# Optimization experiments

Measured on AMD Instinct MI355X. Metric: run time of the kernel, lower is better.

Reference implementation:

```python
import jax, jax.numpy as jnp
import numpy as np

N_NODES = 100000
N_EDGES = 1600000
IN_CH = 128
HEADS = 4
OUT_CH = 32
NEG_SLOPE = 0.2
DIV_WEIGHT = 0.1
EPS_SOFTMAX = 1e-16  # PyG softmax eps
EPS_COS = 1e-8       # F.cosine_similarity eps


def setup_inputs() -> dict:
    key = jax.random.key(0)
    k1, k2, k3, k4, k5 = jax.random.split(key, 5)
    x = jax.random.normal(k1, (N_NODES, IN_CH), dtype=jnp.float32)
    # edge_index with guaranteed no self loops (remove_self_loops becomes a no-op)
    row = jax.random.randint(k2, (N_EDGES,), 0, N_NODES, dtype=jnp.int32)
    off = jax.random.randint(k3, (N_EDGES,), 1, N_NODES, dtype=jnp.int32)
    col = (row + off) % N_NODES
    edge_index = jnp.stack([row, col], axis=0)
    # params (xavier-ish scale)
    W = jax.random.normal(k4, (HEADS * OUT_CH, IN_CH), dtype=jnp.float32) * np.sqrt(2.0 / (IN_CH + HEADS * OUT_CH))
    att = jax.random.normal(k5, (1, HEADS, 2 * OUT_CH), dtype=jnp.float32) * np.sqrt(2.0 / (1 + 2 * OUT_CH))
    bias = jnp.zeros((HEADS * OUT_CH,), dtype=jnp.float32)
    return {"x": x, "edge_index": edge_index, "W": W, "att": att, "bias": bias}


def reference(x, edge_index, W, att, bias):
    N = x.shape[0]
    H = att.shape[1]
    C = att.shape[2] // 2
    idx_dtype = edge_index.dtype
    # add self loops (input has none, so remove_self_loops is a no-op)
    loops = jnp.arange(N, dtype=idx_dtype)
    row = jnp.concatenate([edge_index[0], loops])  # destination
    col = jnp.concatenate([edge_index[1], loops])  # source
    # linear projection -> [N, H, C]
    h = (x @ W.T).reshape(N, H, C)
    # attention logits: (cat(x_i, x_j) * att).sum(-1) == s_i[row] + s_j[col]
    s_i = jnp.einsum('nhc,hc->nh', h, att[0, :, :C])  # [N, H]
    s_j = jnp.einsum('nhc,hc->nh', h, att[0, :, C:])  # [N, H]
    e = s_i[row] + s_j[col]                            # [E, H]
    e = jnp.where(e >= 0, e, NEG_SLOPE * e)            # leaky_relu
    # segment softmax over destination node (row)
    e_max = jax.ops.segment_max(e, row, num_segments=N)
    e_max = jnp.where(jnp.isfinite(e_max), e_max, 0.0)
    e_exp = jnp.exp(e - e_max[row])
    denom = jax.ops.segment_sum(e_exp, row, num_segments=N)
    alpha = e_exp / (denom[row] + EPS_SOFTMAX)         # [E, H]
    # attention diversity loss: mean pairwise cosine sim (zero diagonal)
    gram = alpha.T @ alpha                             # [H, H]
    norms = jnp.sqrt(jnp.diag(gram))
    corr = gram / jnp.maximum(norms[:, None] * norms[None, :], EPS_COS)
    corr = corr * (1.0 - jnp.eye(H, dtype=corr.dtype))
    diversity_loss = jnp.mean(corr) * DIV_WEIGHT
    # weighted message + scatter-add aggregation (dropout p=0 -> identity)
    msg = h[col] * alpha[:, :, None]                   # [E, H, C]
    out = jax.ops.segment_sum(msg, row, num_segments=N)
    out = out.reshape(N, H * C) + bias                 # concat=True
    return out, diversity_loss
```

## Files before the change

kernel.cpp:

```cpp
#include <hip/hip_runtime.h>
#include <math.h>

#define HC     128
#define SLOT   64
#define AGG_BLOCKS 2048
#define NPART  8
#define CHUNKS 256

typedef unsigned int uint32;
typedef short bf16x8 __attribute__((ext_vector_type(8)));
typedef float f32x4 __attribute__((ext_vector_type(4)));

__device__ inline unsigned short f2bf(float f){
  uint32 u = __float_as_uint(f);
  u = (u + 0x7fffu + ((u >> 16) & 1u)) >> 16;
  return (unsigned short)u;
}
__device__ inline uint32 pack_bf2(float a, float b){
  return (uint32)f2bf(a) | ((uint32)f2bf(b) << 16);
}
__device__ inline void lds_fence(){
  asm volatile("s_waitcnt lgkmcnt(0)" ::: "memory");
  __builtin_amdgcn_sched_barrier(0);
}


__global__ __launch_bounds__(256) void k_fill(const int* __restrict__ row, const int* __restrict__ col,
                                              int* cnt, int* bucket, int E, int N){
  int k = blockIdx.x & (NPART-1);
  int c = blockIdx.x >> 3;
  int per  = (E + CHUNKS - 1) / CHUNKS;
  int base = c * per;
  int end  = base + per; if (end > E) end = E;
  int rng  = (N + NPART - 1) / NPART;
  int lo = k * rng, hi = lo + rng;
  for (int i = base + threadIdx.x; i < end; i += 256){
    int d = row[i];
    if (d >= lo && d < hi){
      int pos = atomicAdd(&cnt[d], 1);
      if (pos < SLOT-1) bucket[(size_t)d*SLOT + pos] = col[i];
    }
  }
}


__global__ __launch_bounds__(256) void k_gemm(const float* __restrict__ x, const float* __restrict__ W,
                                              const float* __restrict__ att,
                                              uint32* __restrict__ h_pair,
                                              float* __restrict__ s_i, float* __restrict__ s_j, int N){
  __shared__ __align__(16) unsigned short Blds[128*128];
  int t = threadIdx.x;
  int w = t >> 6, l = t & 63;
  int o = l & 15, lg = l >> 4;
  int n0 = blockIdx.x * 64;

  #pragma unroll
  for (int i = 0; i < 8; ++i){
    int id = t + i*256;
    int r  = id >> 4, ck = id & 15;
    int sw = ck ^ (r & 7);
    float4 b0 = *(const float4*)&W[(size_t)r*128 + ck*8];
    float4 b1 = *(const float4*)&W[(size_t)r*128 + ck*8 + 4];
    bf16x8 pb;
    pb[0]=(short)f2bf(b0.x); pb[1]=(short)f2bf(b0.y); pb[2]=(short)f2bf(b0.z); pb[3]=(short)f2bf(b0.w);
    pb[4]=(short)f2bf(b1.x); pb[5]=(short)f2bf(b1.y); pb[6]=(short)f2bf(b1.z); pb[7]=(short)f2bf(b1.w);
    *(bf16x8*)&Blds[r*128 + sw*8] = pb;
  }

  int arow = n0 + w*16 + o;
  bool rok = (arow < N);
  const float* xr = x + (size_t)arow*128;
  bf16x8 afr[4];
  #pragma unroll
  for (int ks = 0; ks < 4; ++ks){
    float4 a0 = make_float4(0.f,0.f,0.f,0.f), a1 = a0;
    if (rok){
      a0 = *(const float4*)&xr[ks*32 + lg*8];
      a1 = *(const float4*)&xr[ks*32 + lg*8 + 4];
    }
    bf16x8 pa;
    pa[0]=(short)f2bf(a0.x); pa[1]=(short)f2bf(a0.y); pa[2]=(short)f2bf(a0.z); pa[3]=(short)f2bf(a0.w);
    pa[4]=(short)f2bf(a1.x); pa[5]=(short)f2bf(a1.y); pa[6]=(short)f2bf(a1.z); pa[7]=(short)f2bf(a1.w);
    afr[ks] = pa;
  }
  __syncthreads();

  f32x4 acc[8];
  #pragma unroll
  for (int cf = 0; cf < 8; ++cf) acc[cf] = (f32x4){0.f,0.f,0.f,0.f};

  #pragma unroll
  for (int ks = 0; ks < 4; ++ks){
    int ckk = ks*4 + lg;
    #pragma unroll
    for (int cf = 0; cf < 8; ++cf){
      int rb = cf*16 + o;
      bf16x8 bfr = *(const bf16x8*)&Blds[rb*128 + (ckk ^ (rb & 7))*8];
      acc[cf] = __builtin_amdgcn_mfma_f32_16x16x32_bf16(afr[ks], bfr, acc[cf], 0, 0, 0);
    }
  }

  float ai0[4], ai1[4], aj0[4], aj1[4];
  #pragma unroll
  for (int hd = 0; hd < 4; ++hd){
    ai0[hd] = att[hd*64 + o];
    ai1[hd] = att[hd*64 + 16 + o];
    aj0[hd] = att[hd*64 + 32 + o];
    aj1[hd] = att[hd*64 + 48 + o];
  }

  #pragma unroll
  for (int q = 0; q < 4; ++q){
    int node = n0 + w*16 + lg*4 + q;
    float v[8];
    #pragma unroll
    for (int cf = 0; cf < 8; ++cf) v[cf] = acc[cf][q];
    float pi[4], pj[4];
    #pragma unroll
    for (int hd = 0; hd < 4; ++hd){
      pi[hd] = v[2*hd]*ai0[hd] + v[2*hd+1]*ai1[hd];
      pj[hd] = v[2*hd]*aj0[hd] + v[2*hd+1]*aj1[hd];
    }
    #pragma unroll
    for (int sh = 1; sh < 16; sh <<= 1){
      #pragma unroll
      for (int hd = 0; hd < 4; ++hd){
        pi[hd] += __shfl_xor(pi[hd], sh);
        pj[hd] += __shfl_xor(pj[hd], sh);
      }
    }
    if (node < N){
      #pragma unroll
      for (int hd = 0; hd < 4; ++hd)
        h_pair[(size_t)node*64 + hd*16 + o] = pack_bf2(v[2*hd], v[2*hd+1]);
      if (o == 0){
        *(float4*)&s_i[(size_t)node*4] = make_float4(pi[0], pi[1], pi[2], pi[3]);
        *(float4*)&s_j[(size_t)node*4] = make_float4(pj[0], pj[1], pj[2], pj[3]);
      }
    }
  }
}


__global__ __launch_bounds__(256) void k_agg(const uint32* __restrict__ h_pair, const float* __restrict__ s_i,
                                             const float* __restrict__ s_j, const int* __restrict__ cnt,
                                             const int* __restrict__ bucket,
                                             const float* __restrict__ bias, float* __restrict__ out,
                                             float* __restrict__ gram_part, int N){
  __shared__ __align__(16) float al[4][SLOT*4];
  __shared__ int   cs[4][SLOT];
  __shared__ float red[4][10];
  int t = threadIdx.x;
  int w = t >> 6, l = t & 63;
  int g = l >> 4, o = l & 15;
  float b0 = bias[32*g + o];
  float b1 = bias[32*g + 16 + o];
  float ga[10];
  #pragma unroll
  for (int p = 0; p < 10; ++p) ga[p] = 0.f;
  int TW = gridDim.x * 4;

  for (int n = blockIdx.x*4 + w; n < N; n += TW){
    int dc = cnt[n]; if (dc > SLOT-1) dc = SLOT-1;
    int d  = dc + 1;
    float4 si = *(const float4*)&s_i[(size_t)n*4];
    if (l < d){
      int src = (l < dc) ? bucket[(size_t)n*SLOT + l] : n;
      cs[w][l] = src << 6;
      float4 sj = *(const float4*)&s_j[(size_t)src*4];
      float4 e;
      e.x = si.x + sj.x; e.y = si.y + sj.y; e.z = si.z + sj.z; e.w = si.w + sj.w;
      e.x = e.x >= 0.f ? e.x : 0.2f*e.x;
      e.y = e.y >= 0.f ? e.y : 0.2f*e.y;
      e.z = e.z >= 0.f ? e.z : 0.2f*e.z;
      e.w = e.w >= 0.f ? e.w : 0.2f*e.w;
      *(float4*)&al[w][l*4] = e;
    }
    lds_fence();
    float m = -3.4e38f;
    for (int j = o; j < d; j += 16) m = fmaxf(m, al[w][j*4 + g]);
    #pragma unroll
    for (int sh = 1; sh < 16; sh <<= 1) m = fmaxf(m, __shfl_xor(m, sh));
    float sum = 0.f;
    for (int j = o; j < d; j += 16){
      float v = __expf(al[w][j*4 + g] - m);
      al[w][j*4 + g] = v;
      sum += v;
    }
    #pragma unroll
    for (int sh = 1; sh < 16; sh <<= 1) sum += __shfl_xor(sum, sh);
    float r = 1.f/(sum + 1e-16f);
    for (int j = o; j < d; j += 16) al[w][j*4 + g] *= r;
    lds_fence();
    if (l < d){
      float4 a = *(const float4*)&al[w][l*4];
      ga[0] += a.x*a.x; ga[1] += a.x*a.y; ga[2] += a.x*a.z; ga[3] += a.x*a.w;
      ga[4] += a.y*a.y; ga[5] += a.y*a.z; ga[6] += a.y*a.w;
      ga[7] += a.z*a.z; ga[8] += a.z*a.w;
      ga[9] += a.w*a.w;
    }
    float a0 = 0.f, a1 = 0.f;
    const float* alw = &al[w][0];
    const int*   csw = &cs[w][0];
    int j = 0;
    for (; j + 4 <= d; j += 4){
      int   o0 = csw[j+0], o1 = csw[j+1], o2 = csw[j+2], o3 = csw[j+3];
      float w0 = alw[(j+0)*4 + g], w1 = alw[(j+1)*4 + g];
      float w2 = alw[(j+2)*4 + g], w3 = alw[(j+3)*4 + g];
      uint32 v0 = h_pair[(size_t)(uint32)(o0 + l)];
      uint32 v1 = h_pair[(size_t)(uint32)(o1 + l)];
      uint32 v2 = h_pair[(size_t)(uint32)(o2 + l)];
      uint32 v3 = h_pair[(size_t)(uint32)(o3 + l)];
      a0 += w0 * __uint_as_float(v0 << 16);  a1 += w0 * __uint_as_float(v0 & 0xffff0000u);
      a0 += w1 * __uint_as_float(v1 << 16);  a1 += w1 * __uint_as_float(v1 & 0xffff0000u);
      a0 += w2 * __uint_as_float(v2 << 16);  a1 += w2 * __uint_as_float(v2 & 0xffff0000u);
      a0 += w3 * __uint_as_float(v3 << 16);  a1 += w3 * __uint_as_float(v3 & 0xffff0000u);
    }
    for (; j < d; ++j){
      float aw = alw[j*4 + g];
      uint32 v = h_pair[(size_t)(uint32)(csw[j] + l)];
      a0 += aw * __uint_as_float(v << 16);
      a1 += aw * __uint_as_float(v & 0xffff0000u);
    }
    out[(size_t)n*128 + 32*g + o]      = a0 + b0;
    out[(size_t)n*128 + 32*g + 16 + o] = a1 + b1;
    lds_fence();
  }
  __syncthreads();
  #pragma unroll
  for (int p = 0; p < 10; ++p){
    float v = ga[p];
    #pragma unroll
    for (int sh = 1; sh < 64; sh <<= 1) v += __shfl_xor(v, sh);
    ga[p] = v;
  }
  if (l == 0){
    #pragma unroll
    for (int p = 0; p < 10; ++p) red[w][p] = ga[p];
  }
  __syncthreads();
  if (t == 0){
    #pragma unroll
    for (int p = 0; p < 10; ++p)
      gram_part[(size_t)blockIdx.x*10 + p] = red[0][p] + red[1][p] + red[2][p] + red[3][p];
  }
}


__global__ __launch_bounds__(256) void k_final(const float* __restrict__ gram_part, int nparts,
                                               float* __restrict__ loss){
  __shared__ float red[4][10];
  int t = threadIdx.x;
  float acc[10];
  #pragma unroll
  for (int p = 0; p < 10; ++p) acc[p] = 0.f;
  for (int i = t; i < nparts; i += 256){
    #pragma unroll
    for (int p = 0; p < 10; ++p) acc[p] += gram_part[(size_t)i*10 + p];
  }
  #pragma unroll
  for (int p = 0; p < 10; ++p){
    float v = acc[p];
    #pragma unroll
    for (int sh = 1; sh < 64; sh <<= 1) v += __shfl_xor(v, sh);
    acc[p] = v;
  }
  if ((t & 63) == 0){
    #pragma unroll
    for (int p = 0; p < 10; ++p) red[t >> 6][p] = acc[p];
  }
  __syncthreads();
  if (t == 0){
    float gs[10];
    #pragma unroll
    for (int p = 0; p < 10; ++p) gs[p] = red[0][p] + red[1][p] + red[2][p] + red[3][p];
    float G[4][4];
    G[0][0]=gs[0]; G[0][1]=gs[1]; G[0][2]=gs[2]; G[0][3]=gs[3];
    G[1][0]=gs[1]; G[1][1]=gs[4]; G[1][2]=gs[5]; G[1][3]=gs[6];
    G[2][0]=gs[2]; G[2][1]=gs[5]; G[2][2]=gs[7]; G[2][3]=gs[8];
    G[3][0]=gs[3]; G[3][1]=gs[6]; G[3][2]=gs[8]; G[3][3]=gs[9];
    float nr[4];
    for (int i = 0; i < 4; ++i) nr[i] = sqrtf(G[i][i]);
    float ssum = 0.f;
    for (int i = 0; i < 4; ++i)
      for (int j = 0; j < 4; ++j)
        if (i != j) ssum += G[i][j] / fmaxf(nr[i]*nr[j], 1e-8f);
    loss[0] = ssum * (0.1f/16.f);
  }
}


extern "C" void kernel_launch(void* const* d_in, const int* in_sizes, int n_in,
                              void* d_out, int out_size, void* d_ws, size_t ws_size,
                              hipStream_t stream){
  const float* x    = (const float*)d_in[0];
  const int*   edge = (const int*)d_in[1];
  const float* W    = (const float*)d_in[2];
  const float* att  = (const float*)d_in[3];
  const float* bias = (const float*)d_in[4];
  int N = in_sizes[0] / 128;
  int E = in_sizes[1] / 2;
  const int* row = edge;
  const int* col = edge + E;
  float* out  = (float*)d_out;
  float* loss = out + (size_t)N*HC;

  char* wsb = (char*)d_ws;
  size_t off = 0;
  auto alloc = [&](size_t bytes)->void*{
    size_t o = (off + 255) & ~(size_t)255;
    off = o + bytes;
    return (void*)(wsb + o);
  };
  uint32* h_pair   = (uint32*)alloc((size_t)N*64*sizeof(uint32));
  float* s_i       = (float*)alloc((size_t)N*4*sizeof(float));
  float* s_j       = (float*)alloc((size_t)N*4*sizeof(float));
  int*   cnt       = (int*)alloc((size_t)N*sizeof(int));
  int*   bucket    = (int*)alloc((size_t)N*SLOT*sizeof(int));
  float* gram_part = (float*)alloc((size_t)AGG_BLOCKS*10*sizeof(float));
  (void)ws_size; (void)n_in; (void)out_size;

  hipMemsetAsync(cnt, 0, (size_t)N*sizeof(int), stream);
  k_fill<<<CHUNKS*NPART,256,0,stream>>>(row, col, cnt, bucket, E, N);
  int GB = (N+63)/64;
  k_gemm<<<GB,256,0,stream>>>(x, W, att, h_pair, s_i, s_j, N);
  k_agg<<<AGG_BLOCKS,256,0,stream>>>(h_pair, s_i, s_j, cnt, bucket, bias, out, gram_part, N);
  k_final<<<1,256,0,stream>>>(gram_part, AGG_BLOCKS, loss);
}
```

Before: 189.5 us.

## Fuse bucket fill into GEMM kernel and widen aggregation gathers to 8 bytes

The edge bucketing kernel and the projection GEMM are merged into one launch. The first ntiles blocks compute a GEMM tile and then every block processes an edge chunk, which removes a launch and lets the two phases overlap. In aggregation, each half-wave now handles alternate edges and loads 8-byte uint2 pairs of the bf16 features, so there are half as many gather instructions per edge. Odd degrees are padded with a zero-weight edge, the two halves are combined with a cross-half shuffle, and bucket loads and output stores become nontemporal. The cost is extra shuffles and padding logic in the per-node loop.

Measured after the change: 207.4 us. +9.4%, slower.

```diff
diff --git a/kernel.cpp b/kernel.cpp
--- a/kernel.cpp
+++ b/kernel.cpp
@@ -4,10 +4,11 @@
 #define HC     128
 #define SLOT   64
 #define AGG_BLOCKS 2048
+#define PREP_GRID  2048
 #define NPART  8
-#define CHUNKS 256
 
 typedef unsigned int uint32;
+typedef unsigned long long uint64;
 typedef short bf16x8 __attribute__((ext_vector_type(8)));
 typedef float f32x4 __attribute__((ext_vector_type(4)));
 
@@ -25,117 +26,123 @@
 }
 
 
-__global__ __launch_bounds__(256) void k_fill(const int* __restrict__ row, const int* __restrict__ col,
-                                              int* cnt, int* bucket, int E, int N){
-  int k = blockIdx.x & (NPART-1);
-  int c = blockIdx.x >> 3;
-  int per  = (E + CHUNKS - 1) / CHUNKS;
-  int base = c * per;
-  int end  = base + per; if (end > E) end = E;
-  int rng  = (N + NPART - 1) / NPART;
-  int lo = k * rng, hi = lo + rng;
-  for (int i = base + threadIdx.x; i < end; i += 256){
-    int d = row[i];
-    if (d >= lo && d < hi){
-      int pos = atomicAdd(&cnt[d], 1);
-      if (pos < SLOT-1) bucket[(size_t)d*SLOT + pos] = col[i];
-    }
-  }
-}
-
-
-__global__ __launch_bounds__(256) void k_gemm(const float* __restrict__ x, const float* __restrict__ W,
+__global__ __launch_bounds__(256) void k_prep(const float* __restrict__ x, const float* __restrict__ W,
                                               const float* __restrict__ att,
+                                              const int* __restrict__ row, const int* __restrict__ col,
+                                              int* cnt, int* bucket,
                                               uint32* __restrict__ h_pair,
-                                              float* __restrict__ s_i, float* __restrict__ s_j, int N){
+                                              float* __restrict__ s_i, float* __restrict__ s_j,
+                                              int N, int E, int ntiles){
   __shared__ __align__(16) unsigned short Blds[128*128];
   int t = threadIdx.x;
-  int w = t >> 6, l = t & 63;
-  int o = l & 15, lg = l >> 4;
-  int n0 = blockIdx.x * 64;
-
-  #pragma unroll
-  for (int i = 0; i < 8; ++i){
-    int id = t + i*256;
-    int r  = id >> 4, ck = id & 15;
-    int sw = ck ^ (r & 7);
-    float4 b0 = *(const float4*)&W[(size_t)r*128 + ck*8];
-    float4 b1 = *(const float4*)&W[(size_t)r*128 + ck*8 + 4];
-    bf16x8 pb;
-    pb[0]=(short)f2bf(b0.x); pb[1]=(short)f2bf(b0.y); pb[2]=(short)f2bf(b0.z); pb[3]=(short)f2bf(b0.w);
-    pb[4]=(short)f2bf(b1.x); pb[5]=(short)f2bf(b1.y); pb[6]=(short)f2bf(b1.z); pb[7]=(short)f2bf(b1.w);
-    *(bf16x8*)&Blds[r*128 + sw*8] = pb;
-  }
-
-  int arow = n0 + w*16 + o;
-  bool rok = (arow < N);
-  const float* xr = x + (size_t)arow*128;
-  bf16x8 afr[4];
-  #pragma unroll
-  for (int ks = 0; ks < 4; ++ks){
-    float4 a0 = make_float4(0.f,0.f,0.f,0.f), a1 = a0;
-    if (rok){
-      a0 = *(const float4*)&xr[ks*32 + lg*8];
-      a1 = *(const float4*)&xr[ks*32 + lg*8 + 4];
-    }
-    bf16x8 pa;
-    pa[0]=(short)f2bf(a0.x); pa[1]=(short)f2bf(a0.y); pa[2]=(short)f2bf(a0.z); pa[3]=(short)f2bf(a0.w);
-    pa[4]=(short)f2bf(a1.x); pa[5]=(short)f2bf(a1.y); pa[6]=(short)f2bf(a1.z); pa[7]=(short)f2bf(a1.w);
-    afr[ks] = pa;
-  }
-  __syncthreads();
-
-  f32x4 acc[8];
-  #pragma unroll
-  for (int cf = 0; cf < 8; ++cf) acc[cf] = (f32x4){0.f,0.f,0.f,0.f};
-
-  #pragma unroll
-  for (int ks = 0; ks < 4; ++ks){
-    int ckk = ks*4 + lg;
-    #pragma unroll
-    for (int cf = 0; cf < 8; ++cf){
-      int rb = cf*16 + o;
-      bf16x8 bfr = *(const bf16x8*)&Blds[rb*128 + (ckk ^ (rb & 7))*8];
-      acc[cf] = __builtin_amdgcn_mfma_f32_16x16x32_bf16(afr[ks], bfr, acc[cf], 0, 0, 0);
-    }
-  }
-
-  float ai0[4], ai1[4], aj0[4], aj1[4];
-  #pragma unroll
-  for (int hd = 0; hd < 4; ++hd){
-    ai0[hd] = att[hd*64 + o];
-    ai1[hd] = att[hd*64 + 16 + o];
-    aj0[hd] = att[hd*64 + 32 + o];
-    aj1[hd] = att[hd*64 + 48 + o];
-  }
-
-  #pragma unroll
-  for (int q = 0; q < 4; ++q){
-    int node = n0 + w*16 + lg*4 + q;
-    float v[8];
-    #pragma unroll
-    for (int cf = 0; cf < 8; ++cf) v[cf] = acc[cf][q];
-    float pi[4], pj[4];
+  bool hasTile = ((int)blockIdx.x < ntiles);
+
+  if (hasTile){
+    int w = t >> 6, l = t & 63;
+    int o = l & 15, lg = l >> 4;
+    int n0 = blockIdx.x * 64;
+
+    #pragma unroll
+    for (int i = 0; i < 8; ++i){
+      int id = t + i*256;
+      int r  = id >> 4, ck = id & 15;
+      int sw = ck ^ (r & 7);
+      float4 b0 = *(const float4*)&W[(size_t)r*128 + ck*8];
+      float4 b1 = *(const float4*)&W[(size_t)r*128 + ck*8 + 4];
+      bf16x8 pb;
+      pb[0]=(short)f2bf(b0.x); pb[1]=(short)f2bf(b0.y); pb[2]=(short)f2bf(b0.z); pb[3]=(short)f2bf(b0.w);
+      pb[4]=(short)f2bf(b1.x); pb[5]=(short)f2bf(b1.y); pb[6]=(short)f2bf(b1.z); pb[7]=(short)f2bf(b1.w);
+      *(bf16x8*)&Blds[r*128 + sw*8] = pb;
+    }
+
+    int arow = n0 + w*16 + o;
+    bool rok = (arow < N);
+    const float* xr = x + (size_t)arow*128;
+    bf16x8 afr[4];
+    #pragma unroll
+    for (int ks = 0; ks < 4; ++ks){
+      float4 a0 = make_float4(0.f,0.f,0.f,0.f), a1 = a0;
+      if (rok){
+        a0 = *(const float4*)&xr[ks*32 + lg*8];
+        a1 = *(const float4*)&xr[ks*32 + lg*8 + 4];
+      }
+      bf16x8 pa;
+      pa[0]=(short)f2bf(a0.x); pa[1]=(short)f2bf(a0.y); pa[2]=(short)f2bf(a0.z); pa[3]=(short)f2bf(a0.w);
+      pa[4]=(short)f2bf(a1.x); pa[5]=(short)f2bf(a1.y); pa[6]=(short)f2bf(a1.z); pa[7]=(short)f2bf(a1.w);
+      afr[ks] = pa;
+    }
+    __syncthreads();
+
+    f32x4 acc[8];
+    #pragma unroll
+    for (int cf = 0; cf < 8; ++cf) acc[cf] = (f32x4){0.f,0.f,0.f,0.f};
+
+    #pragma unroll
+    for (int ks = 0; ks < 4; ++ks){
+      int ckk = ks*4 + lg;
+      #pragma unroll
+      for (int cf = 0; cf < 8; ++cf){
+        int rb = cf*16 + o;
+        bf16x8 bfr = *(const bf16x8*)&Blds[rb*128 + (ckk ^ (rb & 7))*8];
+        acc[cf] = __builtin_amdgcn_mfma_f32_16x16x32_bf16(afr[ks], bfr, acc[cf], 0, 0, 0);
+      }
+    }
+
+    float ai0[4], ai1[4], aj0[4], aj1[4];
     #pragma unroll
     for (int hd = 0; hd < 4; ++hd){
-      pi[hd] = v[2*hd]*ai0[hd] + v[2*hd+1]*ai1[hd];
-      pj[hd] = v[2*hd]*aj0[hd] + v[2*hd+1]*aj1[hd];
-    }
-    #pragma unroll
-    for (int sh = 1; sh < 16; sh <<= 1){
+      ai0[hd] = att[hd*64 + o];
+      ai1[hd] = att[hd*64 + 16 + o];
+      aj0[hd] = att[hd*64 + 32 + o];
+      aj1[hd] = att[hd*64 + 48 + o];
+    }
+
+    #pragma unroll
+    for (int q = 0; q < 4; ++q){
+      int node = n0 + w*16 + lg*4 + q;
+      float v[8];
+      #pragma unroll
+      for (int cf = 0; cf < 8; ++cf) v[cf] = acc[cf][q];
+      float pi[4], pj[4];
       #pragma unroll
       for (int hd = 0; hd < 4; ++hd){
-        pi[hd] += __shfl_xor(pi[hd], sh);
-        pj[hd] += __shfl_xor(pj[hd], sh);
-      }
-    }
-    if (node < N){
+        pi[hd] = v[2*hd]*ai0[hd] + v[2*hd+1]*ai1[hd];
+        pj[hd] = v[2*hd]*aj0[hd] + v[2*hd+1]*aj1[hd];
+      }
       #pragma unroll
-      for (int hd = 0; hd < 4; ++hd)
-        h_pair[(size_t)node*64 + hd*16 + o] = pack_bf2(v[2*hd], v[2*hd+1]);
-      if (o == 0){
-        *(float4*)&s_i[(size_t)node*4] = make_float4(pi[0], pi[1], pi[2], pi[3]);
-        *(float4*)&s_j[(size_t)node*4] = make_float4(pj[0], pj[1], pj[2], pj[3]);
+      for (int sh = 1; sh < 16; sh <<= 1){
+        #pragma unroll
+        for (int hd = 0; hd < 4; ++hd){
+          pi[hd] += __shfl_xor(pi[hd], sh);
+          pj[hd] += __shfl_xor(pj[hd], sh);
+        }
+      }
+      if (node < N){
+        #pragma unroll
+        for (int hd = 0; hd < 4; ++hd)
+          h_pair[(size_t)node*64 + hd*16 + o] = pack_bf2(v[2*hd], v[2*hd+1]);
+        if (o == 0){
+          *(float4*)&s_i[(size_t)node*4] = make_float4(pi[0], pi[1], pi[2], pi[3]);
+          *(float4*)&s_j[(size_t)node*4] = make_float4(pj[0], pj[1], pj[2], pj[3]);
+        }
+      }
+    }
+  }
+
+  {
+    int k = blockIdx.x & (NPART-1);
+    int c = blockIdx.x >> 3;
+    int CH = PREP_GRID / NPART;
+    int per  = (E + CH - 1) / CH;
+    int base = c * per;
+    int end  = base + per; if (end > E) end = E;
+    int rng  = (N + NPART - 1) / NPART;
+    int lo = k * rng, hi = lo + rng;
+    for (int i = base + t; i < end; i += 256){
+      int d = row[i];
+      if (d >= lo && d < hi){
+        int pos = atomicAdd(&cnt[d], 1);
+        if (pos < SLOT-1) bucket[(size_t)d*SLOT + pos] = col[i];
       }
     }
   }
@@ -150,11 +157,15 @@
   __shared__ __align__(16) float al[4][SLOT*4];
   __shared__ int   cs[4][SLOT];
   __shared__ float red[4][10];
+  const uint2* hp2 = (const uint2*)h_pair;
   int t = threadIdx.x;
   int w = t >> 6, l = t & 63;
   int g = l >> 4, o = l & 15;
-  float b0 = bias[32*g + o];
-  float b1 = bias[32*g + 16 + o];
+  int lw = l & 31, half = l >> 5;
+  int g2 = lw >> 3;
+  int o0 = (2*lw) & 15;
+  int cbase = 32*g2 + (half << 4) + o0;
+  float2 bv = *(const float2*)&bias[cbase];
   float ga[10];
   #pragma unroll
   for (int p = 0; p < 10; ++p) ga[p] = 0.f;
@@ -165,8 +176,8 @@
     int d  = dc + 1;
     float4 si = *(const float4*)&s_i[(size_t)n*4];
     if (l < d){
-      int src = (l < dc) ? bucket[(size_t)n*SLOT + l] : n;
-      cs[w][l] = src << 6;
+      int src = (l < dc) ? __builtin_nontemporal_load(&bucket[(size_t)n*SLOT + l]) : n;
+      cs[w][l] = src << 5;
       float4 sj = *(const float4*)&s_j[(size_t)src*4];
       float4 e;
       e.x = si.x + sj.x; e.y = si.y + sj.y; e.z = si.z + sj.z; e.w = si.w + sj.w;
@@ -175,6 +186,10 @@
       e.z = e.z >= 0.f ? e.z : 0.2f*e.z;
       e.w = e.w >= 0.f ? e.w : 0.2f*e.w;
       *(float4*)&al[w][l*4] = e;
+    }
+    if ((d & 1) && l == d){
+      cs[w][l] = n << 5;
+      *(float4*)&al[w][l*4] = make_float4(0.f,0.f,0.f,0.f);
     }
     lds_fence();
     float m = -3.4e38f;
@@ -199,31 +214,44 @@
       ga[7] += a.z*a.z; ga[8] += a.z*a.w;
       ga[9] += a.w*a.w;
     }
-    float a0 = 0.f, a1 = 0.f;
+    float a0 = 0.f, a1 = 0.f, a2 = 0.f, a3 = 0.f;
     const float* alw = &al[w][0];
     const int*   csw = &cs[w][0];
-    int j = 0;
-    for (; j + 4 <= d; j += 4){
-      int   o0 = csw[j+0], o1 = csw[j+1], o2 = csw[j+2], o3 = csw[j+3];
-      float w0 = alw[(j+0)*4 + g], w1 = alw[(j+1)*4 + g];
-      float w2 = alw[(j+2)*4 + g], w3 = alw[(j+3)*4 + g];
-      uint32 v0 = h_pair[(size_t)(uint32)(o0 + l)];
-      uint32 v1 = h_pair[(size_t)(uint32)(o1 + l)];
-      uint32 v2 = h_pair[(size_t)(uint32)(o2 + l)];
-      uint32 v3 = h_pair[(size_t)(uint32)(o3 + l)];
-      a0 += w0 * __uint_as_float(v0 << 16);  a1 += w0 * __uint_as_float(v0 & 0xffff0000u);
-      a0 += w1 * __uint_as_float(v1 << 16);  a1 += w1 * __uint_as_float(v1 & 0xffff0000u);
-      a0 += w2 * __uint_as_float(v2 << 16);  a1 += w2 * __uint_as_float(v2 & 0xffff0000u);
-      a0 += w3 * __uint_as_float(v3 << 16);  a1 += w3 * __uint_as_float(v3 & 0xffff0000u);
-    }
-    for (; j < d; ++j){
-      float aw = alw[j*4 + g];
-      uint32 v = h_pair[(size_t)(uint32)(csw[j] + l)];
-      a0 += aw * __uint_as_float(v << 16);
-      a1 += aw * __uint_as_float(v & 0xffff0000u);
-    }
-    out[(size_t)n*128 + 32*g + o]      = a0 + b0;
-    out[(size_t)n*128 + 32*g + 16 + o] = a1 + b1;
+    int npair = (d + 1) >> 1;
+    int i = 0;
+    for (; i + 4 <= npair; i += 4){
+      int e0 = 2*i + half, e1 = e0 + 2, e2 = e0 + 4, e3 = e0 + 6;
+      int s0 = csw[e0], s1 = csw[e1], s2 = csw[e2], s3 = csw[e3];
+      float w0 = alw[e0*4 + g2], w1 = alw[e1*4 + g2];
+      float w2 = alw[e2*4 + g2], w3 = alw[e3*4 + g2];
+      uint2 v0 = hp2[(size_t)(uint32)(s0 + lw)];
+      uint2 v1 = hp2[(size_t)(uint32)(s1 + lw)];
+      uint2 v2 = hp2[(size_t)(uint32)(s2 + lw)];
+      uint2 v3 = hp2[(size_t)(uint32)(s3 + lw)];
+      a0 += w0 * __uint_as_float(v0.x << 16);  a1 += w0 * __uint_as_float(v0.x & 0xffff0000u);
+      a2 += w0 * __uint_as_float(v0.y << 16);  a3 += w0 * __uint_as_float(v0.y & 0xffff0000u);
+      a0 += w1 * __uint_as_float(v1.x << 16);  a1 += w1 * __uint_as_float(v1.x & 0xffff0000u);
+      a2 += w1 * __uint_as_float(v1.y << 16);  a3 += w1 * __uint_as_float(v1.y & 0xffff0000u);
+      a0 += w2 * __uint_as_float(v2.x << 16);  a1 += w2 * __uint_as_float(v2.x & 0xffff0000u);
+      a2 += w2 * __uint_as_float(v2.y << 16);  a3 += w2 * __uint_as_float(v2.y & 0xffff0000u);
+      a0 += w3 * __uint_as_float(v3.x << 16);  a1 += w3 * __uint_as_float(v3.x & 0xffff0000u);
+      a2 += w3 * __uint_as_float(v3.y << 16);  a3 += w3 * __uint_as_float(v3.y & 0xffff0000u);
+    }
+    for (; i < npair; ++i){
+      int e = 2*i + half;
+      float aw = alw[e*4 + g2];
+      uint2 v = hp2[(size_t)(uint32)(csw[e] + lw)];
+      a0 += aw * __uint_as_float(v.x << 16);  a1 += aw * __uint_as_float(v.x & 0xffff0000u);
+      a2 += aw * __uint_as_float(v.y << 16);  a3 += aw * __uint_as_float(v.y & 0xffff0000u);
+    }
+    a0 += __shfl_xor(a0, 32);
+    a1 += __shfl_xor(a1, 32);
+    a2 += __shfl_xor(a2, 32);
+    a3 += __shfl_xor(a3, 32);
+    union { float f[2]; uint64 u; } st;
+    st.f[0] = (half ? a1 : a0) + bv.x;
+    st.f[1] = (half ? a3 : a2) + bv.y;
+    __builtin_nontemporal_store(st.u, (uint64*)&out[(size_t)n*128 + cbase]);
     lds_fence();
   }
   __syncthreads();
@@ -321,9 +349,8 @@
   (void)ws_size; (void)n_in; (void)out_size;
 
   hipMemsetAsync(cnt, 0, (size_t)N*sizeof(int), stream);
-  k_fill<<<CHUNKS*NPART,256,0,stream>>>(row, col, cnt, bucket, E, N);
-  int GB = (N+63)/64;
-  k_gemm<<<GB,256,0,stream>>>(x, W, att, h_pair, s_i, s_j, N);
+  int ntiles = (N+63)/64;
+  k_prep<<<PREP_GRID,256,0,stream>>>(x, W, att, row, col, cnt, bucket, h_pair, s_i, s_j, N, E, ntiles);
   k_agg<<<AGG_BLOCKS,256,0,stream>>>(h_pair, s_i, s_j, cnt, bucket, bias, out, gram_part, N);
   k_final<<<1,256,0,stream>>>(gram_part, AGG_BLOCKS, loss);
 }
```
